# Optimization experiments

Hardware: AMD Instinct MI355X
Metric: run time of the kernel (lower is better)

The kernel has to match this reference:

```python
import jax, jax.numpy as jnp
import numpy as np


def setup_inputs() -> dict:
    key = jax.random.key(0)
    k1, k2 = jax.random.split(key)
    B, S, D, E = 4, 4096, 2048, 64
    x = jax.random.normal(k1, (B, S, D), dtype=jnp.float32)
    gate_w = jax.random.normal(k2, (E, D), dtype=jnp.float32) * (1.0 / np.sqrt(D))
    return {"x": x, "gate_w": gate_w, "top_k": 2}


def reference(x, gate_w, top_k):
    # logits = x @ W^T : [B, S, E]
    logits = jnp.einsum("bsd,ed->bse", x, gate_w)
    probs = jax.nn.softmax(logits, axis=-1)
    top_k_probs, top_k_indices = jax.lax.top_k(probs, top_k)
    top_k_probs = top_k_probs / jnp.sum(top_k_probs, axis=-1, keepdims=True)
    return (top_k_probs, top_k_indices, probs)
```

## Files before the change

kernel.cpp:

```cpp
#include <hip/hip_runtime.h>
#include <math.h>


typedef _Float16 half8  __attribute__((ext_vector_type(8)));
typedef float    floatx4 __attribute__((ext_vector_type(4)));

#define NTOK  16384
#define DDIM  2048
#define NE    64

__device__ inline void split8(const float4& a, const float4& b,
                              half8& hi, half8& lo) {
    float f[8] = {a.x, a.y, a.z, a.w, b.x, b.y, b.z, b.w};
#pragma unroll
    for (int j = 0; j < 8; ++j) {
        const _Float16 h = (_Float16)f[j];
        hi[j] = h;
        lo[j] = (_Float16)(f[j] - (float)h);
    }
}

__global__ __launch_bounds__(256) void w_split2(const float* __restrict__ W,
                                                _Float16* __restrict__ img) {
    const int g  = blockIdx.x * 256 + threadIdx.x;
    const int L  = g & 63;
    const int Bk = g >> 6;
    const int h  = Bk & 1;
    const int nt = (Bk >> 1) & 3;
    const int ch = (Bk >> 3) & 1;
    const int s  = (Bk >> 4) & 15;
    const int kk = (Bk >> 8) & 1;
    const int c  = L & 15, q = L >> 4;
    const float* src = W + (size_t)(nt * 16 + c) * DDIM
                         + kk * 1024 + s * 64 + ch * 32 + q * 8;
    const float4 a = *(const float4*)(src);
    const float4 b = *(const float4*)(src + 4);
    half8 hi, lo;
    split8(a, b, hi, lo);
    *(half8*)(img + (size_t)g * 8) = h ? lo : hi;
}

__global__ __launch_bounds__(256, 2) void router_mfma(
    const float* __restrict__ x,
    const _Float16* __restrict__ img,
    float* __restrict__ out)
{
    __shared__ __align__(16) float lg[32 * 68];

    const int tid = threadIdx.x;
    const int L   = tid & 63;
    const int wv  = __builtin_amdgcn_readfirstlane(tid >> 6);
    const int kk  = wv & 1;
    const int tg  = wv >> 1;
    const int c   = L & 15, q = L >> 4;
    const int btok = blockIdx.x * 32;
    const int tok0 = btok + tg * 16;

    const float*    xp = x + (size_t)(tok0 + c) * DDIM + kk * 1024 + q * 8;
    const _Float16* wp = img + (size_t)kk * 131072 + (size_t)L * 8;

    floatx4 acc[4];
#pragma unroll
    for (int nt = 0; nt < 4; ++nt) acc[nt] = (floatx4)0.f;

    float4 xb0[4], xb1[4];
    half8  wb0[16], wb1[16];

    auto LX = [&](int s, float4* xb) {
#pragma unroll
        for (int ch = 0; ch < 2; ++ch) {
            xb[2 * ch + 0] = *(const float4*)(xp + s * 64 + ch * 32);
            xb[2 * ch + 1] = *(const float4*)(xp + s * 64 + ch * 32 + 4);
        }
    };
    auto LW = [&](int s, half8* wb) {
#pragma unroll
        for (int f = 0; f < 16; ++f)
            wb[f] = *(const half8*)(wp + (size_t)s * 8192 + f * 512);
    };
    auto CP = [&](const float4* xb, const half8* wb) {
#pragma unroll
        for (int ch = 0; ch < 2; ++ch) {
            half8 Ah, Al;
            split8(xb[2 * ch], xb[2 * ch + 1], Ah, Al);
#pragma unroll
            for (int nt = 0; nt < 4; ++nt) {
                const half8 Bh = wb[ch * 8 + nt * 2];
                const half8 Bl = wb[ch * 8 + nt * 2 + 1];
                acc[nt] = __builtin_amdgcn_mfma_f32_16x16x32_f16(Ah, Bh, acc[nt], 0, 0, 0);
                acc[nt] = __builtin_amdgcn_mfma_f32_16x16x32_f16(Al, Bh, acc[nt], 0, 0, 0);
                acc[nt] = __builtin_amdgcn_mfma_f32_16x16x32_f16(Ah, Bl, acc[nt], 0, 0, 0);
            }
        }
    };

    LX(0, xb0); LW(0, wb0);
#pragma unroll
    for (int b = 0; b < 16; b += 2) {
        LX(b + 1, xb1); LW(b + 1, wb1);
        CP(xb0, wb0);
        if (b + 2 < 16) { LX(b + 2, xb0); LW(b + 2, wb0); }
        CP(xb1, wb1);
    }

    if (kk == 1) {
#pragma unroll
        for (int nt = 0; nt < 4; ++nt)
#pragma unroll
            for (int r = 0; r < 4; ++r)
                lg[(tg * 16 + q * 4 + r) * 68 + nt * 16 + c] = acc[nt][r];
    }
    __syncthreads();
    if (kk == 0) {
#pragma unroll
        for (int nt = 0; nt < 4; ++nt)
#pragma unroll
            for (int r = 0; r < 4; ++r) {
                const int o = (tg * 16 + q * 4 + r) * 68 + nt * 16 + c;
                lg[o] += acc[nt][r];
            }
    }
    __syncthreads();

    if (tid < 32) {
        const int token = btok + tid;
        float* row = &lg[tid * 68];
        float pr[NE];
#pragma unroll
        for (int e = 0; e < NE; ++e) pr[e] = row[e];

        float m = pr[0];
#pragma unroll
        for (int e = 1; e < NE; ++e) m = fmaxf(m, pr[e]);
        float s = 0.f;
#pragma unroll
        for (int e = 0; e < NE; ++e) { pr[e] = expf(pr[e] - m); s += pr[e]; }
        const float inv = 1.f / s;

        float v1 = -1.f; int i1 = 0;
#pragma unroll
        for (int e = 0; e < NE; ++e) { if (pr[e] > v1) { v1 = pr[e]; i1 = e; } }
        float v2 = -1.f; int i2 = 0;
#pragma unroll
        for (int e = 0; e < NE; ++e) { if (e != i1 && pr[e] > v2) { v2 = pr[e]; i2 = e; } }

        const float ts = v1 + v2;
        float* out_tp = out;
        float* out_ti = out + 2 * NTOK;
        *(float2*)(out_tp + token * 2) = make_float2(v1 / ts, v2 / ts);
        *(float2*)(out_ti + token * 2) = make_float2((float)i1, (float)i2);

#pragma unroll
        for (int e = 0; e < NE; ++e) row[e] = pr[e] * inv;
    }
    __syncthreads();

    {
        float* out_p = out + 4 * NTOK + (size_t)btok * NE;
#pragma unroll
        for (int i = 0; i < 2; ++i) {
            const int f = tid + 256 * i;
            const int r = f >> 4, c4 = f & 15;
            const float4 v = *(const float4*)&lg[r * 68 + 4 * c4];
            *(float4*)(out_p + f * 4) = v;
        }
    }
}

extern "C" void kernel_launch(void* const* d_in, const int* in_sizes, int n_in,
                              void* d_out, int out_size, void* d_ws, size_t ws_size,
                              hipStream_t stream) {
    const float* x = (const float*)d_in[0];
    const float* W = (const float*)d_in[1];
    float* out     = (float*)d_out;
    _Float16* img  = (_Float16*)d_ws;

    w_split2<<<dim3(128), dim3(256), 0, stream>>>(W, img);
    router_mfma<<<dim3(NTOK / 32), dim3(256), 0, stream>>>(x, img, out);
}
```

Baseline: 226.2 us.

## Split K four ways per block over 16 tokens and reduce partials in LDS

Each block now handles 16 tokens, and its four waves each take a quarter of the 2048-wide K dimension. Before, each block handled 32 tokens, with two token groups and a two-way K split. The partial logits from the waves are summed through four LDS slabs, and the weight-image layout is rewritten so each wave reads a contiguous quarter. The main loop is no longer fully unrolled, weight registers are scoped per iteration, and launch bounds are raised to three blocks per CU to cut register pressure and raise occupancy. In exchange, twice as many blocks each reread the weight image, and the LDS reduction step is added.

```diff
diff --git a/kernel.cpp b/kernel.cpp
--- a/kernel.cpp
+++ b/kernel.cpp
@@ -28,11 +28,10 @@
     const int h  = Bk & 1;
     const int nt = (Bk >> 1) & 3;
     const int ch = (Bk >> 3) & 1;
-    const int s  = (Bk >> 4) & 15;
-    const int kk = (Bk >> 8) & 1;
+    const int gs = Bk >> 4;
     const int c  = L & 15, q = L >> 4;
     const float* src = W + (size_t)(nt * 16 + c) * DDIM
-                         + kk * 1024 + s * 64 + ch * 32 + q * 8;
+                         + gs * 64 + ch * 32 + q * 8;
     const float4 a = *(const float4*)(src);
     const float4 b = *(const float4*)(src + 4);
     half8 hi, lo;
@@ -40,31 +39,27 @@
     *(half8*)(img + (size_t)g * 8) = h ? lo : hi;
 }
 
-__global__ __launch_bounds__(256, 2) void router_mfma(
+__global__ __launch_bounds__(256, 3) void router_mfma(
     const float* __restrict__ x,
     const _Float16* __restrict__ img,
     float* __restrict__ out)
 {
-    __shared__ __align__(16) float lg[32 * 68];
+    __shared__ __align__(16) float lg[4 * 16 * 68];
 
     const int tid = threadIdx.x;
     const int L   = tid & 63;
-    const int wv  = __builtin_amdgcn_readfirstlane(tid >> 6);
-    const int kk  = wv & 1;
-    const int tg  = wv >> 1;
+    const int kq  = __builtin_amdgcn_readfirstlane(tid >> 6);
     const int c   = L & 15, q = L >> 4;
-    const int btok = blockIdx.x * 32;
-    const int tok0 = btok + tg * 16;
+    const int btok = blockIdx.x * 16;
 
-    const float*    xp = x + (size_t)(tok0 + c) * DDIM + kk * 1024 + q * 8;
-    const _Float16* wp = img + (size_t)kk * 131072 + (size_t)L * 8;
+    const float*    xp = x + (size_t)(btok + c) * DDIM + kq * 512 + q * 8;
+    const _Float16* wp = img + (size_t)kq * 65536 + (size_t)L * 8;
 
     floatx4 acc[4];
 #pragma unroll
     for (int nt = 0; nt < 4; ++nt) acc[nt] = (floatx4)0.f;
 
-    float4 xb0[4], xb1[4];
-    half8  wb0[16], wb1[16];
+    float4 xA[4], xB[4];
 
     auto LX = [&](int s, float4* xb) {
 #pragma unroll
@@ -94,35 +89,44 @@
         }
     };
 
-    LX(0, xb0); LW(0, wb0);
-#pragma unroll
-    for (int b = 0; b < 16; b += 2) {
-        LX(b + 1, xb1); LW(b + 1, wb1);
-        CP(xb0, wb0);
-        if (b + 2 < 16) { LX(b + 2, xb0); LW(b + 2, wb0); }
-        CP(xb1, wb1);
+    LX(0, xA);
+    LX(1, xB);
+#pragma unroll 1
+    for (int b = 0; b < 6; b += 2) {
+        half8 wA[16], wB[16];
+        LW(b, wA);
+        CP(xA, wA);
+        LX(b + 2, xA);
+        LW(b + 1, wB);
+        CP(xB, wB);
+        LX(b + 3, xB);
+    }
+    {
+        half8 wA[16], wB[16];
+        LW(6, wA); CP(xA, wA);
+        LW(7, wB); CP(xB, wB);
     }
 
-    if (kk == 1) {
+    {
+        float* slab = &lg[kq * 16 * 68];
 #pragma unroll
         for (int nt = 0; nt < 4; ++nt)
 #pragma unroll
             for (int r = 0; r < 4; ++r)
-                lg[(tg * 16 + q * 4 + r) * 68 + nt * 16 + c] = acc[nt][r];
-    }
-    __syncthreads();
-    if (kk == 0) {
-#pragma unroll
-        for (int nt = 0; nt < 4; ++nt)
-#pragma unroll
-            for (int r = 0; r < 4; ++r) {
-                const int o = (tg * 16 + q * 4 + r) * 68 + nt * 16 + c;
-                lg[o] += acc[nt][r];
-            }
+                slab[(q * 4 + r) * 68 + nt * 16 + c] = acc[nt][r];
     }
     __syncthreads();
 
-    if (tid < 32) {
+#pragma unroll
+    for (int i = 0; i < 4; ++i) {
+        const int e = tid + 256 * i;
+        const int r = e >> 6, col = e & 63;
+        const int o = r * 68 + col;
+        lg[o] = (lg[o] + lg[1088 + o]) + (lg[2176 + o] + lg[3264 + o]);
+    }
+    __syncthreads();
+
+    if (tid < 16) {
         const int token = btok + tid;
         float* row = &lg[tid * 68];
         float pr[NE];
@@ -157,13 +161,9 @@
 
     {
         float* out_p = out + 4 * NTOK + (size_t)btok * NE;
-#pragma unroll
-        for (int i = 0; i < 2; ++i) {
-            const int f = tid + 256 * i;
-            const int r = f >> 4, c4 = f & 15;
-            const float4 v = *(const float4*)&lg[r * 68 + 4 * c4];
-            *(float4*)(out_p + f * 4) = v;
-        }
+        const int r = tid >> 4, c4 = tid & 15;
+        const float4 v = *(const float4*)&lg[r * 68 + 4 * c4];
+        *(float4*)(out_p + tid * 4) = v;
     }
 }
 
@@ -176,5 +176,5 @@
     _Float16* img  = (_Float16*)d_ws;
 
     w_split2<<<dim3(128), dim3(256), 0, stream>>>(W, img);
-    router_mfma<<<dim3(NTOK / 32), dim3(256), 0, stream>>>(x, img, out);
+    router_mfma<<<dim3(NTOK / 16), dim3(256), 0, stream>>>(x, img, out);
 }
```

Result: faster. 206.1 us (-8.9%).

## Stage split weight tiles in LDS via global_load_lds double buffering

Applied to the files above, without the earlier changes.

Weight hi/lo fp16 tiles were previously loaded by every wave straight from global memory into registers. They are now staged cooperatively into double-buffered LDS with direct global-to-LDS loads, and each wave reads its B fragments from LDS. The K split across waves changes from two contiguous halves to interleaved 32-element chunks over 32 steps, with a matching relayout of the weight image. The aim is to stop the two token-group waves from loading the same weight data redundantly and to shrink the register footprint. In exchange it adds a block barrier every step, LDS traffic, and manual waitcnt handling.

```diff
diff --git a/kernel.cpp b/kernel.cpp
--- a/kernel.cpp
+++ b/kernel.cpp
@@ -8,6 +8,8 @@
 #define NTOK  16384
 #define DDIM  2048
 #define NE    64
+#define TPB   32
+#define NSTEP 32
 
 __device__ inline void split8(const float4& a, const float4& b,
                               half8& hi, half8& lo) {
@@ -20,24 +22,30 @@
     }
 }
 
-__global__ __launch_bounds__(256) void w_split2(const float* __restrict__ W,
+typedef const __attribute__((address_space(1))) unsigned int* as1_u32p;
+typedef __attribute__((address_space(3))) unsigned int*       as3_u32p;
+
+__device__ inline void gload_lds16(const void* g, void* l) {
+    __builtin_amdgcn_global_load_lds((as1_u32p)g, (as3_u32p)l, 16, 0, 0);
+}
+
+__global__ __launch_bounds__(256) void w_split3(const float* __restrict__ W,
                                                 _Float16* __restrict__ img) {
     const int g  = blockIdx.x * 256 + threadIdx.x;
     const int L  = g & 63;
-    const int Bk = g >> 6;
-    const int h  = Bk & 1;
-    const int nt = (Bk >> 1) & 3;
-    const int ch = (Bk >> 3) & 1;
-    const int s  = (Bk >> 4) & 15;
-    const int kk = (Bk >> 8) & 1;
+    const int B  = g >> 6;
+    const int nt = B & 3;
+    const int hl = (B >> 2) & 1;
+    const int kh = (B >> 3) & 1;
+    const int st = B >> 4;
     const int c  = L & 15, q = L >> 4;
     const float* src = W + (size_t)(nt * 16 + c) * DDIM
-                         + kk * 1024 + s * 64 + ch * 32 + q * 8;
+                         + st * 64 + kh * 32 + q * 8;
     const float4 a = *(const float4*)(src);
     const float4 b = *(const float4*)(src + 4);
     half8 hi, lo;
     split8(a, b, hi, lo);
-    *(half8*)(img + (size_t)g * 8) = h ? lo : hi;
+    *(half8*)(img + (size_t)g * 8) = hl ? lo : hi;
 }
 
 __global__ __launch_bounds__(256, 2) void router_mfma(
@@ -45,65 +53,78 @@
     const _Float16* __restrict__ img,
     float* __restrict__ out)
 {
-    __shared__ __align__(16) float lg[32 * 68];
+    __shared__ __align__(16) _Float16 tiles[2 * 8192];
+    __shared__ __align__(16) float lg[TPB * 68];
 
     const int tid = threadIdx.x;
     const int L   = tid & 63;
     const int wv  = __builtin_amdgcn_readfirstlane(tid >> 6);
-    const int kk  = wv & 1;
+    const int kh  = wv & 1;
     const int tg  = wv >> 1;
     const int c   = L & 15, q = L >> 4;
-    const int btok = blockIdx.x * 32;
-    const int tok0 = btok + tg * 16;
-
-    const float*    xp = x + (size_t)(tok0 + c) * DDIM + kk * 1024 + q * 8;
-    const _Float16* wp = img + (size_t)kk * 131072 + (size_t)L * 8;
+    const int btok = blockIdx.x * TPB;
+
+    const float* xp = x + (size_t)(btok + tg * 16 + c) * DDIM + kh * 32 + q * 8;
+
+    int boff[4][2];
+#pragma unroll
+    for (int nt = 0; nt < 4; ++nt)
+#pragma unroll
+        for (int hl = 0; hl < 2; ++hl)
+            boff[nt][hl] = (((kh * 2 + hl) * 4 + nt) * 64 + L) * 8;
 
     floatx4 acc[4];
 #pragma unroll
     for (int nt = 0; nt < 4; ++nt) acc[nt] = (floatx4)0.f;
 
-    float4 xb0[4], xb1[4];
-    half8  wb0[16], wb1[16];
-
-    auto LX = [&](int s, float4* xb) {
-#pragma unroll
-        for (int ch = 0; ch < 2; ++ch) {
-            xb[2 * ch + 0] = *(const float4*)(xp + s * 64 + ch * 32);
-            xb[2 * ch + 1] = *(const float4*)(xp + s * 64 + ch * 32 + 4);
+    auto stage_w = [&](int sel, int t) {
+        const char* src = (const char*)img + (size_t)t * 16384;
+#pragma unroll
+        for (int r = 0; r < 4; ++r) {
+            const int gi0 = r * 256 + wv * 64;
+            gload_lds16(src + (size_t)(gi0 + L) * 16,
+                        &tiles[sel * 8192 + gi0 * 8]);
         }
     };
-    auto LW = [&](int s, half8* wb) {
-#pragma unroll
-        for (int f = 0; f < 16; ++f)
-            wb[f] = *(const half8*)(wp + (size_t)s * 8192 + f * 512);
-    };
-    auto CP = [&](const float4* xb, const half8* wb) {
-#pragma unroll
-        for (int ch = 0; ch < 2; ++ch) {
-            half8 Ah, Al;
-            split8(xb[2 * ch], xb[2 * ch + 1], Ah, Al);
-#pragma unroll
-            for (int nt = 0; nt < 4; ++nt) {
-                const half8 Bh = wb[ch * 8 + nt * 2];
-                const half8 Bl = wb[ch * 8 + nt * 2 + 1];
-                acc[nt] = __builtin_amdgcn_mfma_f32_16x16x32_f16(Ah, Bh, acc[nt], 0, 0, 0);
-                acc[nt] = __builtin_amdgcn_mfma_f32_16x16x32_f16(Al, Bh, acc[nt], 0, 0, 0);
-                acc[nt] = __builtin_amdgcn_mfma_f32_16x16x32_f16(Ah, Bl, acc[nt], 0, 0, 0);
-            }
+
+    auto compute = [&](int sel, const float4& xa, const float4& xb) {
+        const _Float16* base = &tiles[sel * 8192];
+        half8 Ah, Al;
+        split8(xa, xb, Ah, Al);
+#pragma unroll
+        for (int nt = 0; nt < 4; ++nt) {
+            const half8 Bh = *(const half8*)(base + boff[nt][0]);
+            const half8 Bl = *(const half8*)(base + boff[nt][1]);
+            acc[nt] = __builtin_amdgcn_mfma_f32_16x16x32_f16(Ah, Bh, acc[nt], 0, 0, 0);
+            acc[nt] = __builtin_amdgcn_mfma_f32_16x16x32_f16(Al, Bh, acc[nt], 0, 0, 0);
+            acc[nt] = __builtin_amdgcn_mfma_f32_16x16x32_f16(Ah, Bl, acc[nt], 0, 0, 0);
         }
     };
 
-    LX(0, xb0); LW(0, wb0);
-#pragma unroll
-    for (int b = 0; b < 16; b += 2) {
-        LX(b + 1, xb1); LW(b + 1, wb1);
-        CP(xb0, wb0);
-        if (b + 2 < 16) { LX(b + 2, xb0); LW(b + 2, wb0); }
-        CP(xb1, wb1);
-    }
-
-    if (kk == 1) {
+    float4 pxa, pxb;
+    {
+        stage_w(0, 0);
+        __builtin_amdgcn_sched_barrier(0);
+        pxa = *(const float4*)(xp);
+        pxb = *(const float4*)(xp + 4);
+        asm volatile("s_waitcnt vmcnt(2) lgkmcnt(0)" ::: "memory");
+        __builtin_amdgcn_s_barrier();
+    }
+
+    for (int t = 0; t < NSTEP - 1; ++t) {
+        stage_w((t + 1) & 1, t + 1);
+        __builtin_amdgcn_sched_barrier(0);
+        const float4 nxa = *(const float4*)(xp + (t + 1) * 64);
+        const float4 nxb = *(const float4*)(xp + (t + 1) * 64 + 4);
+        compute(t & 1, pxa, pxb);
+        asm volatile("s_waitcnt vmcnt(2) lgkmcnt(0)" ::: "memory");
+        __builtin_amdgcn_s_barrier();
+        pxa = nxa; pxb = nxb;
+    }
+    compute((NSTEP - 1) & 1, pxa, pxb);
+    __syncthreads();
+
+    if (kh == 1) {
 #pragma unroll
         for (int nt = 0; nt < 4; ++nt)
 #pragma unroll
@@ -111,7 +132,7 @@
                 lg[(tg * 16 + q * 4 + r) * 68 + nt * 16 + c] = acc[nt][r];
     }
     __syncthreads();
-    if (kk == 0) {
+    if (kh == 0) {
 #pragma unroll
         for (int nt = 0; nt < 4; ++nt)
 #pragma unroll
@@ -122,7 +143,7 @@
     }
     __syncthreads();
 
-    if (tid < 32) {
+    if (tid < TPB) {
         const int token = btok + tid;
         float* row = &lg[tid * 68];
         float pr[NE];
@@ -175,6 +196,6 @@
     float* out     = (float*)d_out;
     _Float16* img  = (_Float16*)d_ws;
 
-    w_split2<<<dim3(128), dim3(256), 0, stream>>>(W, img);
-    router_mfma<<<dim3(NTOK / 32), dim3(256), 0, stream>>>(x, img, out);
-}
+    w_split3<<<dim3(128), dim3(256), 0, stream>>>(W, img);
+    router_mfma<<<dim3(NTOK / TPB), dim3(256), 0, stream>>>(x, img, out);
+}
```

Result: faster. 209.0 us (-7.6%).

## Split-K router GEMM with LDS-staged split weights and separate softmax pass

Applied to the files above, without the earlier changes.

Replaces the global-memory fp16 hi/lo weight image with per-block conversion of a 512-wide K slice of W into LDS. Each 512-thread block covers 256 tokens over that slice, and the four K-split partials are written to a workspace. A second kernel sums the partials and does the softmax and top-2. The aim is to cut repeated global weight loads per token tile and to raise parallelism. In exchange it adds extra partial-sum traffic (4×16384×64 floats) and an extra launch, and 128KB of LDS per block limits occupancy.

```diff
diff --git a/kernel.cpp b/kernel.cpp
--- a/kernel.cpp
+++ b/kernel.cpp
@@ -3,11 +3,15 @@
 
 
 typedef _Float16 half8  __attribute__((ext_vector_type(8)));
+typedef _Float16 half4  __attribute__((ext_vector_type(4)));
 typedef float    floatx4 __attribute__((ext_vector_type(4)));
 
-#define NTOK  16384
-#define DDIM  2048
-#define NE    64
+#define NTOK   16384
+#define DDIM   2048
+#define NE     64
+#define KSPLIT 4
+#define KC     512
+#define PSTRIDE (NTOK * NE)
 
 __device__ inline void split8(const float4& a, const float4& b,
                               half8& hi, half8& lo) {
@@ -20,105 +24,129 @@
     }
 }
 
-__global__ __launch_bounds__(256) void w_split2(const float* __restrict__ W,
-                                                _Float16* __restrict__ img) {
-    const int g  = blockIdx.x * 256 + threadIdx.x;
-    const int L  = g & 63;
-    const int Bk = g >> 6;
-    const int h  = Bk & 1;
-    const int nt = (Bk >> 1) & 3;
-    const int ch = (Bk >> 3) & 1;
-    const int s  = (Bk >> 4) & 15;
-    const int kk = (Bk >> 8) & 1;
-    const int c  = L & 15, q = L >> 4;
-    const float* src = W + (size_t)(nt * 16 + c) * DDIM
-                         + kk * 1024 + s * 64 + ch * 32 + q * 8;
-    const float4 a = *(const float4*)(src);
-    const float4 b = *(const float4*)(src + 4);
-    half8 hi, lo;
-    split8(a, b, hi, lo);
-    *(half8*)(img + (size_t)g * 8) = h ? lo : hi;
-}
-
-__global__ __launch_bounds__(256, 2) void router_mfma(
+__device__ inline void split4(const float4& a, half4& hi, half4& lo) {
+    float f[4] = {a.x, a.y, a.z, a.w};
+#pragma unroll
+    for (int j = 0; j < 4; ++j) {
+        const _Float16 h = (_Float16)f[j];
+        hi[j] = h;
+        lo[j] = (_Float16)(f[j] - (float)h);
+    }
+}
+
+__global__ __launch_bounds__(512, 2) void router_a(
     const float* __restrict__ x,
-    const _Float16* __restrict__ img,
+    const float* __restrict__ W,
+    float* __restrict__ partial)
+{
+    __shared__ __align__(16) _Float16 wlds[65536];
+
+    const int tid = threadIdx.x;
+    const int L   = tid & 63;
+    const int wv  = __builtin_amdgcn_readfirstlane(tid >> 6);
+    const int c   = L & 15, q = L >> 4;
+    const int tile = blockIdx.x & 63;
+    const int kc   = blockIdx.x >> 6;
+    const int tok_wave = tile * 256 + wv * 32;
+
+#pragma unroll
+    for (int r = 0; r < 16; ++r) {
+        const int i = r * 512 + tid;
+        const int e = i >> 7, f = i & 127;
+        const int s = f >> 3, o = f & 7;
+        const float4 w4 = *(const float4*)(W + (size_t)e * DDIM + kc * KC + f * 4);
+        half4 hi, lo; split4(w4, hi, lo);
+        *(half4*)(wlds + ((s * 2 + 0) * 64 + e) * 32 + o * 4) = hi;
+        *(half4*)(wlds + ((s * 2 + 1) * 64 + e) * 32 + o * 4) = lo;
+    }
+    __syncthreads();
+
+    floatx4 acc[2][4];
+#pragma unroll
+    for (int sub = 0; sub < 2; ++sub)
+#pragma unroll
+        for (int nt = 0; nt < 4; ++nt) acc[sub][nt] = (floatx4)0.f;
+
+    const float* xp0 = x + (size_t)(tok_wave + c) * DDIM + kc * KC + q * 8;
+    const float* xp1 = xp0 + 16 * DDIM;
+
+    float4 xc[2][2], xn[2][2];
+    xc[0][0] = *(const float4*)(xp0);
+    xc[0][1] = *(const float4*)(xp0 + 4);
+    xc[1][0] = *(const float4*)(xp1);
+    xc[1][1] = *(const float4*)(xp1 + 4);
+
+#pragma unroll 1
+    for (int s = 0; s < 16; ++s) {
+        if (s + 1 < 16) {
+            xn[0][0] = *(const float4*)(xp0 + (s + 1) * 32);
+            xn[0][1] = *(const float4*)(xp0 + (s + 1) * 32 + 4);
+            xn[1][0] = *(const float4*)(xp1 + (s + 1) * 32);
+            xn[1][1] = *(const float4*)(xp1 + (s + 1) * 32 + 4);
+        }
+        half8 B[4][2];
+#pragma unroll
+        for (int nt = 0; nt < 4; ++nt)
+#pragma unroll
+            for (int hl = 0; hl < 2; ++hl)
+                B[nt][hl] = *(const half8*)(wlds + ((s * 2 + hl) * 64 + nt * 16 + c) * 32 + q * 8);
+#pragma unroll
+        for (int sub = 0; sub < 2; ++sub) {
+            half8 Ah, Al;
+            split8(xc[sub][0], xc[sub][1], Ah, Al);
+#pragma unroll
+            for (int nt = 0; nt < 4; ++nt) {
+                acc[sub][nt] = __builtin_amdgcn_mfma_f32_16x16x32_f16(Ah, B[nt][0], acc[sub][nt], 0, 0, 0);
+                acc[sub][nt] = __builtin_amdgcn_mfma_f32_16x16x32_f16(Al, B[nt][0], acc[sub][nt], 0, 0, 0);
+                acc[sub][nt] = __builtin_amdgcn_mfma_f32_16x16x32_f16(Ah, B[nt][1], acc[sub][nt], 0, 0, 0);
+            }
+        }
+        if (s + 1 < 16) {
+#pragma unroll
+            for (int sub = 0; sub < 2; ++sub)
+#pragma unroll
+                for (int j = 0; j < 2; ++j) xc[sub][j] = xn[sub][j];
+        }
+    }
+
+    __syncthreads();
+    float* scratch = (float*)wlds + wv * 2048;
+#pragma unroll
+    for (int sub = 0; sub < 2; ++sub)
+#pragma unroll
+        for (int nt = 0; nt < 4; ++nt)
+#pragma unroll
+            for (int r = 0; r < 4; ++r)
+                scratch[(sub * 16 + q * 4 + r) * 64 + nt * 16 + c] = acc[sub][nt][r];
+    float* pp = partial + (size_t)kc * PSTRIDE + (size_t)tok_wave * 64;
+#pragma unroll
+    for (int it = 0; it < 8; ++it) {
+        const int idx = it * 64 + L;
+        *(float4*)(pp + idx * 4) = *(const float4*)(scratch + idx * 4);
+    }
+}
+
+__global__ __launch_bounds__(256) void router_b(
+    const float* __restrict__ partial,
     float* __restrict__ out)
 {
     __shared__ __align__(16) float lg[32 * 68];
 
-    const int tid = threadIdx.x;
-    const int L   = tid & 63;
-    const int wv  = __builtin_amdgcn_readfirstlane(tid >> 6);
-    const int kk  = wv & 1;
-    const int tg  = wv >> 1;
-    const int c   = L & 15, q = L >> 4;
+    const int tid  = threadIdx.x;
     const int btok = blockIdx.x * 32;
-    const int tok0 = btok + tg * 16;
-
-    const float*    xp = x + (size_t)(tok0 + c) * DDIM + kk * 1024 + q * 8;
-    const _Float16* wp = img + (size_t)kk * 131072 + (size_t)L * 8;
-
-    floatx4 acc[4];
-#pragma unroll
-    for (int nt = 0; nt < 4; ++nt) acc[nt] = (floatx4)0.f;
-
-    float4 xb0[4], xb1[4];
-    half8  wb0[16], wb1[16];
-
-    auto LX = [&](int s, float4* xb) {
-#pragma unroll
-        for (int ch = 0; ch < 2; ++ch) {
-            xb[2 * ch + 0] = *(const float4*)(xp + s * 64 + ch * 32);
-            xb[2 * ch + 1] = *(const float4*)(xp + s * 64 + ch * 32 + 4);
-        }
-    };
-    auto LW = [&](int s, half8* wb) {
-#pragma unroll
-        for (int f = 0; f < 16; ++f)
-            wb[f] = *(const half8*)(wp + (size_t)s * 8192 + f * 512);
-    };
-    auto CP = [&](const float4* xb, const half8* wb) {
-#pragma unroll
-        for (int ch = 0; ch < 2; ++ch) {
-            half8 Ah, Al;
-            split8(xb[2 * ch], xb[2 * ch + 1], Ah, Al);
-#pragma unroll
-            for (int nt = 0; nt < 4; ++nt) {
-                const half8 Bh = wb[ch * 8 + nt * 2];
-                const half8 Bl = wb[ch * 8 + nt * 2 + 1];
-                acc[nt] = __builtin_amdgcn_mfma_f32_16x16x32_f16(Ah, Bh, acc[nt], 0, 0, 0);
-                acc[nt] = __builtin_amdgcn_mfma_f32_16x16x32_f16(Al, Bh, acc[nt], 0, 0, 0);
-                acc[nt] = __builtin_amdgcn_mfma_f32_16x16x32_f16(Ah, Bl, acc[nt], 0, 0, 0);
-            }
-        }
-    };
-
-    LX(0, xb0); LW(0, wb0);
-#pragma unroll
-    for (int b = 0; b < 16; b += 2) {
-        LX(b + 1, xb1); LW(b + 1, wb1);
-        CP(xb0, wb0);
-        if (b + 2 < 16) { LX(b + 2, xb0); LW(b + 2, wb0); }
-        CP(xb1, wb1);
-    }
-
-    if (kk == 1) {
-#pragma unroll
-        for (int nt = 0; nt < 4; ++nt)
-#pragma unroll
-            for (int r = 0; r < 4; ++r)
-                lg[(tg * 16 + q * 4 + r) * 68 + nt * 16 + c] = acc[nt][r];
-    }
-    __syncthreads();
-    if (kk == 0) {
-#pragma unroll
-        for (int nt = 0; nt < 4; ++nt)
-#pragma unroll
-            for (int r = 0; r < 4; ++r) {
-                const int o = (tg * 16 + q * 4 + r) * 68 + nt * 16 + c;
-                lg[o] += acc[nt][r];
-            }
+
+#pragma unroll
+    for (int i = 0; i < 2; ++i) {
+        const int idx = i * 256 + tid;
+        const float* p0 = partial + (size_t)btok * 64 + idx * 4;
+        const float4 a = *(const float4*)(p0);
+        const float4 b = *(const float4*)(p0 + PSTRIDE);
+        const float4 cc = *(const float4*)(p0 + 2 * (size_t)PSTRIDE);
+        const float4 d = *(const float4*)(p0 + 3 * (size_t)PSTRIDE);
+        const int row = idx >> 4, c4 = idx & 15;
+        *(float4*)(&lg[row * 68 + c4 * 4]) =
+            make_float4(a.x + b.x + cc.x + d.x, a.y + b.y + cc.y + d.y,
+                        a.z + b.z + cc.z + d.z, a.w + b.w + cc.w + d.w);
     }
     __syncthreads();
 
@@ -173,8 +201,8 @@
     const float* x = (const float*)d_in[0];
     const float* W = (const float*)d_in[1];
     float* out     = (float*)d_out;
-    _Float16* img  = (_Float16*)d_ws;
-
-    w_split2<<<dim3(128), dim3(256), 0, stream>>>(W, img);
-    router_mfma<<<dim3(NTOK / 32), dim3(256), 0, stream>>>(x, img, out);
-}
+    float* pp      = (float*)d_ws;
+
+    router_a<<<dim3(64 * KSPLIT), dim3(512), 0, stream>>>(x, W, pp);
+    router_b<<<dim3(NTOK / 32), dim3(256), 0, stream>>>(pp, out);
+}
```

After: 210.2 us. 7.0% less time.
